# Kernel optimization log

Measured on AMD Instinct MI355X. Metric: run time of the kernel, lower is better.

The kernel has to match this reference:

```python
import jax, jax.numpy as jnp
import numpy as np
from jax import lax

B, T, I, H, O = 2048, 512, 1, 64, 1


def setup_inputs() -> dict:
    key = jax.random.key(0)
    ks = jax.random.split(key, 7)
    stdv = 1.0 / np.sqrt(H)
    return {
        "x": jax.random.normal(ks[0], (B, T, I), dtype=jnp.float32),
        "w_ih": jax.random.uniform(ks[1], (4 * H, I), jnp.float32, -stdv, stdv),
        "w_hh": jax.random.uniform(ks[2], (4 * H, H), jnp.float32, -stdv, stdv),
        "b_ih": jax.random.uniform(ks[3], (4 * H,), jnp.float32, -stdv, stdv),
        "b_hh": jax.random.uniform(ks[4], (4 * H,), jnp.float32, -stdv, stdv),
        "w_fc": jax.random.uniform(ks[5], (O, H), jnp.float32, -stdv, stdv),
        "b_fc": jax.random.uniform(ks[6], (O,), jnp.float32, -stdv, stdv),
    }


def reference(x, w_ih, w_hh, b_ih, b_hh, w_fc, b_fc):
    # x: [B, T, I] (batch_first). Precompute input contribution to gates for all t.
    xT = jnp.swapaxes(x, 0, 1)                                  # [T, B, I]
    x_gates = jnp.einsum("tbi,gi->tbg", xT, w_ih) + b_ih + b_hh  # [T, B, 4H]

    def step(carry, xg):
        h, c = carry
        gates = xg + h @ w_hh.T                                  # [B, 4H]
        i, f, g, o = jnp.split(gates, 4, axis=-1)                # PyTorch gate order i,f,g,o
        i = jax.nn.sigmoid(i)
        f = jax.nn.sigmoid(f)
        g = jnp.tanh(g)
        o = jax.nn.sigmoid(o)
        c = f * c + i * g
        h = o * jnp.tanh(c)
        return (h, c), h

    h0 = jnp.zeros((x.shape[0], w_hh.shape[1]), x.dtype)
    c0 = jnp.zeros_like(h0)
    _, hs = lax.scan(step, (h0, c0), x_gates)                    # hs: [T, B, H]
    hs = jnp.swapaxes(hs, 0, 1)                                  # [B, T, H]
    return hs @ w_fc.T + b_fc                                    # [B, T, O]
```

## Files before the change

### kernel.cpp

```cpp
#include <hip/hip_runtime.h>

#define T_STEPS 512
#define HSTR 72
#define XSTRIDE 520
#define OSTRIDE 513
#define NB 8

typedef _Float16 half8v __attribute__((ext_vector_type(8)));
typedef _Float16 half4v __attribute__((ext_vector_type(4)));
typedef float f32x4 __attribute__((ext_vector_type(4)));

#define K1 1.442695041f
#define K2 2.885390082f

__device__ __forceinline__ float ex2(float x) {
#if __has_builtin(__builtin_amdgcn_exp2f)
    return __builtin_amdgcn_exp2f(x);
#else
    return exp2f(x);
#endif
}
__device__ __forceinline__ float rcp_fast(float x) {
#if __has_builtin(__builtin_amdgcn_rcpf)
    return __builtin_amdgcn_rcpf(x);
#else
    return 1.0f / x;
#endif
}

__device__ __forceinline__ float out_dot(half8v a0, half8v a1,
                                         const float* wfc0, const float* wfc1) {
    float s = 0.f;
#pragma unroll
    for (int j = 0; j < 8; ++j) s = fmaf((float)a0[j], wfc0[j], s);
#pragma unroll
    for (int j = 0; j < 8; ++j) s = fmaf((float)a1[j], wfc1[j], s);
    s += __shfl_xor(s, 16);
    s += __shfl_xor(s, 32);
    return s;
}

__global__ __launch_bounds__(256, 1) void lstm_kernel(
    const float* __restrict__ x, const float* __restrict__ w_ih,
    const float* __restrict__ w_hh, const float* __restrict__ b_ih,
    const float* __restrict__ b_hh, const float* __restrict__ w_fc,
    const float* __restrict__ b_fc, float* __restrict__ out)
{
    __shared__ __align__(16) _Float16 hbuf[2][8 * HSTR];
    __shared__ __align__(16) _Float16 xls[NB * XSTRIDE];
    __shared__ __align__(16) float ols[NB * OSTRIDE];

    const int tid  = threadIdx.x;
    const int w    = tid >> 6;
    const int lane = tid & 63;
    const int q    = lane >> 4;
    const int c    = lane & 15;
    const int hq   = q >> 1;
    const int xbase = 4 * (q & 1);
    const int bat0  = xbase + 2 * hq;
    const int b0   = blockIdx.x * NB;

    for (int i = tid; i < NB * 128; i += 256) {
        int b  = i >> 7;
        int t4 = i & 127;
        float4 v = *(const float4*)(x + (size_t)(b0 + b) * T_STEPS + t4 * 4);
        half4v hv;
        hv[0] = (_Float16)v.x; hv[1] = (_Float16)v.y;
        hv[2] = (_Float16)v.z; hv[3] = (_Float16)v.w;
        *(half4v*)(&xls[b * XSTRIDE + t4 * 4]) = hv;
    }
    for (int i = tid; i < 2 * 8 * HSTR / 2; i += 256) ((int*)hbuf)[i] = 0;

    const float sK[4] = { -K1, -K1, K2, -K1 };
    half8v bfrag[4][2];
    float biasS[4], wihS[4];
#pragma unroll
    for (int n = 0; n < 4; ++n) {
        int g = 64 * n + 16 * w + c;
        biasS[n] = (b_ih[g] + b_hh[g]) * sK[n];
        wihS[n]  = w_ih[g] * sK[n];
#pragma unroll
        for (int kk = 0; kk < 2; ++kk) {
            const float* wp = w_hh + g * 64 + 32 * kk + 8 * q;
            float4 lo  = *(const float4*)(wp);
            float4 hi4 = *(const float4*)(wp + 4);
            half8v f;
            f[0] = (_Float16)(lo.x  * sK[n]); f[1] = (_Float16)(lo.y  * sK[n]);
            f[2] = (_Float16)(lo.z  * sK[n]); f[3] = (_Float16)(lo.w  * sK[n]);
            f[4] = (_Float16)(hi4.x * sK[n]); f[5] = (_Float16)(hi4.y * sK[n]);
            f[6] = (_Float16)(hi4.z * sK[n]); f[7] = (_Float16)(hi4.w * sK[n]);
            bfrag[n][kk] = f;
        }
    }

    float wfc0[8], wfc1[8];
#pragma unroll
    for (int j = 0; j < 8; ++j) { wfc0[j] = w_fc[8 * q + j]; wfc1[j] = w_fc[32 + 8 * q + j]; }
    const float bfc = b_fc[0];

    float cs[2] = {0.f, 0.f};

    __syncthreads();

    half8v sa0 = {}, sa1 = {};

    for (int tq = 0; tq < 128; ++tq) {
        float xq[4][4];
#pragma unroll
        for (int r = 0; r < 4; ++r) {
            half4v hx = *(const half4v*)(&xls[(xbase + r) * XSTRIDE + tq * 4]);
            xq[r][0] = (float)hx[0]; xq[r][1] = (float)hx[1];
            xq[r][2] = (float)hx[2]; xq[r][3] = (float)hx[3];
        }

#pragma unroll
        for (int dt = 0; dt < 4; ++dt) {
            const int t  = tq * 4 + dt;
            const int rb = t & 1;
            const _Float16* hrd = hbuf[rb];

            const _Float16* hp = hrd + (c & 7) * HSTR + 8 * q;
            half8v a0 = *(const half8v*)(hp);
            half8v a1 = *(const half8v*)(hp + 32);

            if (dt == w) { sa0 = a0; sa1 = a1; }

            f32x4 acc[4];
#pragma unroll
            for (int n = 0; n < 4; ++n) {
                f32x4 a;
                a[0] = fmaf(xq[0][dt], wihS[n], biasS[n]);
                a[1] = fmaf(xq[1][dt], wihS[n], biasS[n]);
                a[2] = fmaf(xq[2][dt], wihS[n], biasS[n]);
                a[3] = fmaf(xq[3][dt], wihS[n], biasS[n]);
                acc[n] = __builtin_amdgcn_mfma_f32_16x16x32_f16(a0, bfrag[n][0], a, 0, 0, 0);
                acc[n] = __builtin_amdgcn_mfma_f32_16x16x32_f16(a1, bfrag[n][1], acc[n], 0, 0, 0);
            }

            float v[4][2];
#pragma unroll
            for (int n = 0; n < 4; ++n) {
                v[n][0] = hq ? acc[n][2] : acc[n][0];
                v[n][1] = hq ? acc[n][3] : acc[n][1];
            }

            _Float16* hwr = hbuf[rb ^ 1];
#pragma unroll
            for (int rr = 0; rr < 2; ++rr) {
                float A  = ex2(v[0][rr]);
                float B  = ex2(v[2][rr]);
                float ig = (B - 1.0f) * rcp_fast((1.0f + A) * (1.0f + B));
                float rf = rcp_fast(1.0f + ex2(v[1][rr]));
                cs[rr] = fmaf(cs[rr], rf, ig);
                float cc = fminf(fmaxf(cs[rr], -15.f), 15.f);
                float Ao = ex2(v[3][rr]);
                float C  = ex2(cc * K2);
                float h  = (C - 1.0f) * rcp_fast((1.0f + Ao) * (1.0f + C));
                hwr[(bat0 + rr) * HSTR + 16 * w + c] = (_Float16)h;
            }
            __syncthreads();
        }

        {
            int st = tq * 4 + w;
            if (st > 0) {
                float s = out_dot(sa0, sa1, wfc0, wfc1);
                if (lane < NB) ols[lane * OSTRIDE + (st - 1)] = s + bfc;
            }
        }
    }

    if (w == 3) {
        const _Float16* hp = hbuf[0] + (c & 7) * HSTR + 8 * q;
        half8v a0 = *(const half8v*)(hp);
        half8v a1 = *(const half8v*)(hp + 32);
        float s = out_dot(a0, a1, wfc0, wfc1);
        if (lane < NB) ols[lane * OSTRIDE + (T_STEPS - 1)] = s + bfc;
    }
    __syncthreads();

    for (int i = tid; i < NB * T_STEPS; i += 256) {
        int b = i >> 9;
        int t = i & (T_STEPS - 1);
        out[(size_t)(b0 + b) * T_STEPS + t] = ols[b * OSTRIDE + t];
    }
}

extern "C" void kernel_launch(void* const* d_in, const int* in_sizes, int n_in,
                              void* d_out, int out_size, void* d_ws, size_t ws_size,
                              hipStream_t stream) {
    const float* x    = (const float*)d_in[0];
    const float* w_ih = (const float*)d_in[1];
    const float* w_hh = (const float*)d_in[2];
    const float* b_ih = (const float*)d_in[3];
    const float* b_hh = (const float*)d_in[4];
    const float* w_fc = (const float*)d_in[5];
    const float* b_fc = (const float*)d_in[6];
    float* out = (float*)d_out;
    hipLaunchKernelGGL(lstm_kernel, dim3(2048 / NB), dim3(256), 0, stream,
                       x, w_ih, w_hh, b_ih, b_hh, w_fc, b_fc, out);
}
```

Measured before the change: 272.9 us.

## Halve batches per block and compute one LSTM cell per lane

```diff
diff --git a/kernel.cpp b/kernel.cpp
--- a/kernel.cpp
+++ b/kernel.cpp
@@ -1,10 +1,10 @@
 #include <hip/hip_runtime.h>
 
 #define T_STEPS 512
-#define HSTR 72
+#define HSTR 80
 #define XSTRIDE 520
 #define OSTRIDE 513
-#define NB 8
+#define NB 4
 
 typedef _Float16 half8v __attribute__((ext_vector_type(8)));
 typedef _Float16 half4v __attribute__((ext_vector_type(4)));
@@ -46,7 +46,7 @@
     const float* __restrict__ b_hh, const float* __restrict__ w_fc,
     const float* __restrict__ b_fc, float* __restrict__ out)
 {
-    __shared__ __align__(16) _Float16 hbuf[2][8 * HSTR];
+    __shared__ __align__(16) _Float16 hbuf[2][NB * HSTR];
     __shared__ __align__(16) _Float16 xls[NB * XSTRIDE];
     __shared__ __align__(16) float ols[NB * OSTRIDE];
 
@@ -55,9 +55,6 @@
     const int lane = tid & 63;
     const int q    = lane >> 4;
     const int c    = lane & 15;
-    const int hq   = q >> 1;
-    const int xbase = 4 * (q & 1);
-    const int bat0  = xbase + 2 * hq;
     const int b0   = blockIdx.x * NB;
 
     for (int i = tid; i < NB * 128; i += 256) {
@@ -69,7 +66,7 @@
         hv[2] = (_Float16)v.z; hv[3] = (_Float16)v.w;
         *(half4v*)(&xls[b * XSTRIDE + t4 * 4]) = hv;
     }
-    for (int i = tid; i < 2 * 8 * HSTR / 2; i += 256) ((int*)hbuf)[i] = 0;
+    for (int i = tid; i < 2 * NB * HSTR / 2; i += 256) ((int*)hbuf)[i] = 0;
 
     const float sK[4] = { -K1, -K1, K2, -K1 };
     half8v bfrag[4][2];
@@ -98,20 +95,17 @@
     for (int j = 0; j < 8; ++j) { wfc0[j] = w_fc[8 * q + j]; wfc1[j] = w_fc[32 + 8 * q + j]; }
     const float bfc = b_fc[0];
 
-    float cs[2] = {0.f, 0.f};
+    const bool qb0 = q & 1, qb1 = q & 2;
+
+    float cs = 0.f;
+    const f32x4 zeroq = {0.f, 0.f, 0.f, 0.f};
 
     __syncthreads();
 
     half8v sa0 = {}, sa1 = {};
 
     for (int tq = 0; tq < 128; ++tq) {
-        float xq[4][4];
-#pragma unroll
-        for (int r = 0; r < 4; ++r) {
-            half4v hx = *(const half4v*)(&xls[(xbase + r) * XSTRIDE + tq * 4]);
-            xq[r][0] = (float)hx[0]; xq[r][1] = (float)hx[1];
-            xq[r][2] = (float)hx[2]; xq[r][3] = (float)hx[3];
-        }
+        half4v xh = *(const half4v*)(&xls[q * XSTRIDE + tq * 4]);
 
 #pragma unroll
         for (int dt = 0; dt < 4; ++dt) {
@@ -119,44 +113,43 @@
             const int rb = t & 1;
             const _Float16* hrd = hbuf[rb];
 
-            const _Float16* hp = hrd + (c & 7) * HSTR + 8 * q;
+            const _Float16* hp = hrd + (c & 3) * HSTR + 8 * q;
             half8v a0 = *(const half8v*)(hp);
             half8v a1 = *(const half8v*)(hp + 32);
 
             if (dt == w) { sa0 = a0; sa1 = a1; }
 
+            const float xv = (float)xh[dt];
+            float xb[4];
+#pragma unroll
+            for (int n = 0; n < 4; ++n) xb[n] = fmaf(xv, wihS[n], biasS[n]);
+
             f32x4 acc[4];
 #pragma unroll
             for (int n = 0; n < 4; ++n) {
-                f32x4 a;
-                a[0] = fmaf(xq[0][dt], wihS[n], biasS[n]);
-                a[1] = fmaf(xq[1][dt], wihS[n], biasS[n]);
-                a[2] = fmaf(xq[2][dt], wihS[n], biasS[n]);
-                a[3] = fmaf(xq[3][dt], wihS[n], biasS[n]);
-                acc[n] = __builtin_amdgcn_mfma_f32_16x16x32_f16(a0, bfrag[n][0], a, 0, 0, 0);
-                acc[n] = __builtin_amdgcn_mfma_f32_16x16x32_f16(a1, bfrag[n][1], acc[n], 0, 0, 0);
+                acc[n] = __builtin_amdgcn_mfma_f32_16x16x32_f16(a1, bfrag[n][1], zeroq, 0, 0, 0);
+                acc[n] = __builtin_amdgcn_mfma_f32_16x16x32_f16(a0, bfrag[n][0], acc[n], 0, 0, 0);
             }
 
-            float v[4][2];
+            float v[4];
 #pragma unroll
             for (int n = 0; n < 4; ++n) {
-                v[n][0] = hq ? acc[n][2] : acc[n][0];
-                v[n][1] = hq ? acc[n][3] : acc[n][1];
+                float lo = qb0 ? acc[n][1] : acc[n][0];
+                float hi = qb0 ? acc[n][3] : acc[n][2];
+                v[n] = (qb1 ? hi : lo) + xb[n];
             }
 
-            _Float16* hwr = hbuf[rb ^ 1];
-#pragma unroll
-            for (int rr = 0; rr < 2; ++rr) {
-                float A  = ex2(v[0][rr]);
-                float B  = ex2(v[2][rr]);
+            {
+                float A  = ex2(v[0]);
+                float B  = ex2(v[2]);
                 float ig = (B - 1.0f) * rcp_fast((1.0f + A) * (1.0f + B));
-                float rf = rcp_fast(1.0f + ex2(v[1][rr]));
-                cs[rr] = fmaf(cs[rr], rf, ig);
-                float cc = fminf(fmaxf(cs[rr], -15.f), 15.f);
-                float Ao = ex2(v[3][rr]);
+                float rf = rcp_fast(1.0f + ex2(v[1]));
+                cs = fmaf(cs, rf, ig);
+                float cc = fminf(fmaxf(cs, -15.f), 15.f);
+                float Ao = ex2(v[3]);
                 float C  = ex2(cc * K2);
                 float h  = (C - 1.0f) * rcp_fast((1.0f + Ao) * (1.0f + C));
-                hwr[(bat0 + rr) * HSTR + 16 * w + c] = (_Float16)h;
+                hbuf[rb ^ 1][q * HSTR + 16 * w + c] = (_Float16)h;
             }
             __syncthreads();
         }
@@ -171,7 +164,7 @@
     }
 
     if (w == 3) {
-        const _Float16* hp = hbuf[0] + (c & 7) * HSTR + 8 * q;
+        const _Float16* hp = hbuf[0] + (c & 3) * HSTR + 8 * q;
         half8v a0 = *(const half8v*)(hp);
         half8v a1 = *(const half8v*)(hp + 32);
         float s = out_dot(a0, a1, wfc0, wfc1);
```

Result: slower. 296.4 us (+8.6%).
